# Kernel tuning notes

Measured on AMD Instinct MI355X. Metric: run time of the kernel, lower is better.

Reference implementation:

```python
import jax, jax.numpy as jnp
import numpy as np

B, M, N, D = 1, 128, 256, 256   # batch, msa rows, residues, node dim
DE = 128                        # edge (pair) dim
H, DH = 8, 64                   # heads, dim_head
INNER = H * DH


def setup_inputs() -> dict:
    key = jax.random.key(0)
    ks = jax.random.split(key, 10)
    s = 0.02
    return {
        "x": jax.random.normal(ks[0], (B, M, N, D), jnp.float32),
        "edges": jax.random.normal(ks[1], (B, N, N, DE), jnp.float32),
        "mask": jnp.ones((B, M, N), dtype=bool),
        "ln_g": jnp.ones((D,), jnp.float32),
        "ln_b": jnp.zeros((D,), jnp.float32),
        "Wq": jax.random.normal(ks[2], (D, INNER), jnp.float32) * s,
        "Wkv": jax.random.normal(ks[3], (D, 2 * INNER), jnp.float32) * s,
        "Wg": jax.random.normal(ks[4], (D, INNER), jnp.float32) * s,
        "bg": jnp.ones((INNER,), jnp.float32),
        "Wo": jax.random.normal(ks[5], (INNER, D), jnp.float32) * s,
        "bo": jnp.zeros((D,), jnp.float32),
        "Wb": jax.random.normal(ks[6], (DE, H), jnp.float32) * s,
    }


def reference(x, edges, mask, ln_g, ln_b, Wq, Wkv, Wg, bg, Wo, bo, Wb):
    b, m, n, d = x.shape
    scale = DH ** -0.5
    # LayerNorm over node dim (biased variance, eps=1e-5 as torch default)
    mu = x.mean(-1, keepdims=True)
    var = x.var(-1, keepdims=True)
    xn = (x - mu) / jnp.sqrt(var + 1e-5) * ln_g + ln_b

    # pair bias: [b, h, i, j], shared across MSA rows
    bias = jnp.einsum('bijc,ch->bhij', edges, Wb)

    # projections, split heads: [b, m, n, h, dh]
    q = jnp.einsum('bmnd,de->bmne', xn, Wq).reshape(b, m, n, H, DH) * scale
    kv = jnp.einsum('bmnd,de->bmne', xn, Wkv)
    k = kv[..., :INNER].reshape(b, m, n, H, DH)
    v = kv[..., INNER:].reshape(b, m, n, H, DH)

    # tied queries: mean over MSA rows (global_query_attn, tie_dim=m)
    qm = q.mean(axis=1)  # [b, n, h, dh]
    dots = jnp.einsum('bihd,bmjhd->bmhij', qm, k) + bias[:, None]  # [b,m,h,i,j]

    pair_mask = mask[:, :, None, :, None] & mask[:, :, None, None, :]
    neg = -jnp.finfo(dots.dtype).max
    dots = jnp.where(pair_mask, dots, neg)
    attn = jax.nn.softmax(dots, axis=-1)

    out = jnp.einsum('bmhij,bmjhd->bmihd', attn, v).reshape(b, m, n, INNER)
    gates = jax.nn.sigmoid(jnp.einsum('bmnd,de->bmne', xn, Wg) + bg)
    out = out * gates
    return jnp.einsum('bmne,ed->bmnd', out, Wo) + bo
```

## Files before the change

kernel.cpp:

```cpp
#include <hip/hip_runtime.h>
#include <stdint.h>


#define DEV __device__ __forceinline__

typedef __attribute__((ext_vector_type(8))) short bf16x8;
typedef __attribute__((ext_vector_type(4))) float f32x4;

DEV short f2bf(float f) {
  union { float f; uint32_t u; } v; v.f = f;
  uint32_t r = v.u + 0x7fffu + ((v.u >> 16) & 1u);
  return (short)(r >> 16);
}
DEV float bf2f(short s) {
  union { uint32_t u; float f; } v; v.u = ((uint32_t)(uint16_t)s) << 16;
  return v.f;
}

#define GLDS16(gp, lp) __builtin_amdgcn_global_load_lds( \
    (__attribute__((address_space(1))) void*)(gp),       \
    (__attribute__((address_space(3))) void*)(lp), 16, 0, 0)

__global__ __launch_bounds__(256) void k_ln(const float* __restrict__ x,
                                            const float* __restrict__ g,
                                            const float* __restrict__ b,
                                            short* __restrict__ xn) {
  int wave = threadIdx.x >> 6, lane = threadIdx.x & 63;
  long row = (long)blockIdx.x * 4 + wave;
  const float* xr = x + row * 256;
  float4 v = ((const float4*)xr)[lane];
  float s = v.x + v.y + v.z + v.w;
  float sq = v.x*v.x + v.y*v.y + v.z*v.z + v.w*v.w;
#pragma unroll
  for (int o = 1; o < 64; o <<= 1) { s += __shfl_xor(s, o); sq += __shfl_xor(sq, o); }
  float mu = s * (1.f/256.f);
  float var = sq * (1.f/256.f) - mu*mu;
  float rstd = rsqrtf(var + 1e-5f);
  float4 gg = ((const float4*)g)[lane];
  float4 bb = ((const float4*)b)[lane];
  short4 o4;
  o4.x = f2bf((v.x-mu)*rstd*gg.x + bb.x);
  o4.y = f2bf((v.y-mu)*rstd*gg.y + bb.y);
  o4.z = f2bf((v.z-mu)*rstd*gg.z + bb.z);
  o4.w = f2bf((v.w-mu)*rstd*gg.w + bb.w);
  ((short4*)(xn + row * 256))[lane] = o4;
}

__global__ __launch_bounds__(256) void k_wt(const float* __restrict__ Wq,
                                            const float* __restrict__ Wkv,
                                            const float* __restrict__ Wg,
                                            const float* __restrict__ Wo,
                                            short* __restrict__ WT,
                                            short* __restrict__ WoT) {
  int idx = blockIdx.x * 256 + threadIdx.x;
  if (idx < 2048 * 256) {
    int n = idx >> 8, k = idx & 255;
    float v;
    if (n < 512)       v = Wq[k * 512 + n];
    else if (n < 1536) v = Wkv[k * 1024 + (n - 512)];
    else               v = Wg[k * 512 + (n - 1536)];
    WT[idx] = f2bf(v);
  } else {
    int j = idx - 2048 * 256;
    int k = j & 511;
    WoT[j] = f2bf(Wo[k * 256 + (j >> 9)]);
  }
}

__global__ __launch_bounds__(256) void k_bias(const float* __restrict__ edges,
                                              const float* __restrict__ Wb,
                                              float* __restrict__ biasF) {
  int pair = blockIdx.x * 4 + (threadIdx.x >> 6);
  int lane = threadIdx.x & 63;
  const float* e = edges + (long)pair * 128;
  float a0 = e[lane], a1 = e[lane + 64];
  float acc[8];
#pragma unroll
  for (int h = 0; h < 8; ++h)
    acc[h] = a0 * Wb[lane * 8 + h] + a1 * Wb[(lane + 64) * 8 + h];
#pragma unroll
  for (int o = 1; o < 64; o <<= 1) {
#pragma unroll
    for (int h = 0; h < 8; ++h) acc[h] += __shfl_xor(acc[h], o);
  }
  if (lane == 0) {
    int i = pair >> 8, j = pair & 255;
    long base = ((long)(i >> 4) * 16 + (j >> 4)) * 256 +
                (((i >> 2) & 3) * 16 + (j & 15)) * 4 + (i & 3);
#pragma unroll
    for (int h = 0; h < 8; ++h) biasF[(long)h * 65536 + base] = acc[h];
  }
}

__global__ __launch_bounds__(1024) void k_xbar(const short* __restrict__ xn,
                                               float* __restrict__ xbar) {
  __shared__ float red[3][256];
  int i = blockIdx.x;
  int d = threadIdx.x & 255, mc = threadIdx.x >> 8;
  const short* p = xn + (long)mc * 32 * 65536 + (long)i * 256 + d;
  float s = 0.f;
#pragma unroll 8
  for (int mm = 0; mm < 32; ++mm) s += bf2f(p[(long)mm * 65536]);
  if (mc) red[mc - 1][d] = s;
  __syncthreads();
  if (mc == 0)
    xbar[i * 256 + d] = (s + red[0][d] + red[1][d] + red[2][d]) * (1.f / 128.f);
}

__global__ __launch_bounds__(512) void k_qmg(const float* __restrict__ xbar,
                                             const short* __restrict__ WT,
                                             short* __restrict__ qm) {
  int i = blockIdx.x;
  int e = threadIdx.x;
  const float* xb = xbar + i * 256;
  float acc = 0.f;
  for (int d = 0; d < 256; d += 8) {
    bf16x8 w = *(const bf16x8*)&WT[e * 256 + d];
#pragma unroll
    for (int t = 0; t < 8; ++t) acc += xb[d + t] * bf2f(w[t]);
  }
  qm[((e >> 6) * 256 + i) * 64 + (e & 63)] = f2bf(acc * 0.125f);
}

__global__ __launch_bounds__(512, 4) void k_attn(const short* __restrict__ xn,
                                                 const short* __restrict__ WT,
                                                 const short* __restrict__ qm,
                                                 const float* __restrict__ biasF,
                                                 const float* __restrict__ bg,
                                                 short* __restrict__ outA) {
  __shared__ short kL[256 * 64];
  __shared__ short vL[64 * 256];
  __shared__ short pL[8 * 16 * 64];
  int h = blockIdx.x, m = blockIdx.y;
  int tid = threadIdx.x;
  int wave = tid >> 6, lane = tid & 63;
  int quad = lane >> 4, l15 = lane & 15;
  int l7 = l15 & 7;

  short* WL = kL;
  int rW0 = tid >> 2;
  int gW0 = ((tid & 3) ^ ((rW0 >> 1) & 3)) * 8;
  int rW1 = (512 + tid) >> 2;
  int gW1 = (((512 + tid) & 3) ^ ((rW1 >> 1) & 3)) * 8;
  long wg0 = ((long)(512 * ((rW0 >> 6) + 1) + h * 64 + (rW0 & 63))) * 256;
  long wg1 = ((long)(512 * ((rW1 >> 6) + 1) + h * 64 + (rW1 & 63))) * 256;

#define WSTAGE(buf, kc) do {                                                   \
    int k0_ = (kc) * 32;                                                       \
    GLDS16(WT + wg0 + k0_ + gW0, &WL[(buf) * 6144 + tid * 8]);                 \
    if (tid < 256) GLDS16(WT + wg1 + k0_ + gW1, &WL[(buf) * 6144 + (512 + tid) * 8]); \
  } while (0)

  const short* xp0 = xn + ((long)m * 256 + wave * 32 + l15) * 256 + quad * 8;
  const short* xp1 = xp0 + 16 * 256;

  f32x4 akT[2][4] = {};
  f32x4 av[2][4] = {};
  f32x4 ag[2][4] = {};

  WSTAGE(0, 0);
  bf16x8 xf[2], xnx[2];
  xf[0] = *(const bf16x8*)xp0;
  xf[1] = *(const bf16x8*)xp1;
  for (int kc = 0; kc < 8; ++kc) {
    int cur = kc & 1;
    __syncthreads();
    if (kc < 7) {
      WSTAGE(1 - cur, kc + 1);
      xnx[0] = *(const bf16x8*)(xp0 + (kc + 1) * 32);
      xnx[1] = *(const bf16x8*)(xp1 + (kc + 1) * 32);
    }
#pragma unroll
    for (int tj = 0; tj < 4; ++tj) {
      int rk = tj * 16 + l15;
      int rv = 64 + rk;
      int rg = 128 + rk;
      bf16x8 wk = *(const bf16x8*)&WL[cur * 6144 + rk * 32 + ((quad ^ ((rk >> 1) & 3)) * 8)];
      bf16x8 wv = *(const bf16x8*)&WL[cur * 6144 + rv * 32 + ((quad ^ ((rv >> 1) & 3)) * 8)];
      bf16x8 wg = *(const bf16x8*)&WL[cur * 6144 + rg * 32 + ((quad ^ ((rg >> 1) & 3)) * 8)];
#pragma unroll
      for (int ti = 0; ti < 2; ++ti) {
        akT[ti][tj] = __builtin_amdgcn_mfma_f32_16x16x32_bf16(wk, xf[ti], akT[ti][tj], 0, 0, 0);
        av[ti][tj]  = __builtin_amdgcn_mfma_f32_16x16x32_bf16(xf[ti], wv, av[ti][tj], 0, 0, 0);
        ag[ti][tj]  = __builtin_amdgcn_mfma_f32_16x16x32_bf16(xf[ti], wg, ag[ti][tj], 0, 0, 0);
      }
    }
    xf[0] = xnx[0]; xf[1] = xnx[1];
  }
  __syncthreads();

#undef WSTAGE

#pragma unroll
  for (int ti = 0; ti < 2; ++ti)
#pragma unroll
    for (int tj = 0; tj < 4; ++tj) {
      int j = wave * 32 + ti * 16 + l15;
      int gd = tj * 2 + (quad >> 1);
      short4 pk;
      pk.x = f2bf(akT[ti][tj][0]); pk.y = f2bf(akT[ti][tj][1]);
      pk.z = f2bf(akT[ti][tj][2]); pk.w = f2bf(akT[ti][tj][3]);
      *(short4*)&kL[j * 64 + ((gd ^ (j & 7)) * 8) + (quad & 1) * 4] = pk;
      int d = tj * 16 + l15;
      int j0 = wave * 32 + ti * 16 + quad * 4;
      int jg = j0 >> 3;
      short4 pv;
      pv.x = f2bf(av[ti][tj][0]); pv.y = f2bf(av[ti][tj][1]);
      pv.z = f2bf(av[ti][tj][2]); pv.w = f2bf(av[ti][tj][3]);
      *(short4*)&vL[d * 256 + ((jg ^ (d & 7)) * 8) + (j0 & 7)] = pv;
    }

  const short* qmh = qm + h * (256 * 64);
  bf16x8 aq[2][2];
#pragma unroll
  for (int ti = 0; ti < 2; ++ti)
#pragma unroll
    for (int ks = 0; ks < 2; ++ks)
      aq[ti][ks] = *(const bf16x8*)&qmh[(wave * 32 + ti * 16 + l15) * 64 + ks * 32 + quad * 8];
  float bgv[4];
#pragma unroll
  for (int td = 0; td < 4; ++td) bgv[td] = bg[h * 64 + td * 16 + l15];

  f32x4 o[2][4] = {};
  float lrow[2][4] = {};
  const float* bF = biasF + ((long)h * 16 + wave * 2) * 16 * 256 + lane * 4;

  __syncthreads();

  for (int jc = 0; jc < 4; ++jc) {
    f32x4 s[2][4];
#pragma unroll
    for (int ti = 0; ti < 2; ++ti)
#pragma unroll
      for (int tj = 0; tj < 4; ++tj)
        s[ti][tj] = *(const f32x4*)&bF[((long)ti * 16 + jc * 4 + tj) * 256];
#pragma unroll
    for (int tj = 0; tj < 4; ++tj) {
      int jrow = jc * 64 + tj * 16 + l15;
      bf16x8 b0 = *(const bf16x8*)&kL[jrow * 64 + ((quad ^ l7) * 8)];
      bf16x8 b1 = *(const bf16x8*)&kL[jrow * 64 + (((4 + quad) ^ l7) * 8)];
#pragma unroll
      for (int ti = 0; ti < 2; ++ti) {
        s[ti][tj] = __builtin_amdgcn_mfma_f32_16x16x32_bf16(aq[ti][0], b0, s[ti][tj], 0, 0, 0);
        s[ti][tj] = __builtin_amdgcn_mfma_f32_16x16x32_bf16(aq[ti][1], b1, s[ti][tj], 0, 0, 0);
      }
    }
#pragma unroll
    for (int ti = 0; ti < 2; ++ti) {
#pragma unroll
      for (int r = 0; r < 4; ++r) {
        int rloc = quad * 4 + r;
#pragma unroll
        for (int tj = 0; tj < 4; ++tj) {
          float p = __expf(s[ti][tj][r]);
          lrow[ti][r] += p;
          int col = tj * 16 + l15;
          int slot = (col >> 3) ^ (rloc & 7);
          pL[wave * 1024 + rloc * 64 + slot * 8 + (col & 7)] = f2bf(p);
        }
      }
      bf16x8 ap0 = *(const bf16x8*)&pL[wave * 1024 + l15 * 64 + ((quad ^ l7) * 8)];
      bf16x8 ap1 = *(const bf16x8*)&pL[wave * 1024 + l15 * 64 + (((4 + quad) ^ l7) * 8)];
#pragma unroll
      for (int td = 0; td < 4; ++td) {
        int drow = td * 16 + l15;
        bf16x8 bv0 = *(const bf16x8*)&vL[drow * 256 + (jc * 8 + (quad ^ l7)) * 8];
        bf16x8 bv1 = *(const bf16x8*)&vL[drow * 256 + (jc * 8 + ((4 + quad) ^ l7)) * 8];
        o[ti][td] = __builtin_amdgcn_mfma_f32_16x16x32_bf16(ap0, bv0, o[ti][td], 0, 0, 0);
        o[ti][td] = __builtin_amdgcn_mfma_f32_16x16x32_bf16(ap1, bv1, o[ti][td], 0, 0, 0);
      }
    }
  }

#pragma unroll
  for (int ti = 0; ti < 2; ++ti)
#pragma unroll
    for (int r = 0; r < 4; ++r) {
      float l = lrow[ti][r];
#pragma unroll
      for (int off = 1; off < 16; off <<= 1) l += __shfl_xor(l, off);
      float inv = 1.f / l;
      int i = wave * 32 + ti * 16 + quad * 4 + r;
      long rowoff = (long)m * 256 + i;
#pragma unroll
      for (int td = 0; td < 4; ++td) {
        int dh = td * 16 + l15;
        float gv = 1.f / (1.f + __expf(-(ag[ti][td][r] + bgv[td])));
        outA[rowoff * 512 + h * 64 + dh] = f2bf(o[ti][td][r] * inv * gv);
      }
    }
}

__global__ __launch_bounds__(256, 3) void k_out(const short* __restrict__ A,
                                                const short* __restrict__ B,
                                                float* __restrict__ out,
                                                const float* __restrict__ bo) {
  __shared__ short As[2][128 * 32];
  __shared__ short Bs[2][128 * 32];
  int tid = threadIdx.x;
  int wave = tid >> 6, lane = tid & 63;
  int quad = lane >> 4, l15 = lane & 15;
  long row0 = (long)blockIdx.y * 128;
  int col0 = blockIdx.x * 128;
  int wi = (wave >> 1) * 64, wj = (wave & 1) * 64;
  f32x4 acc[4][4] = {};
  const short* Ab = A + row0 * 512;
  const short* Bb = B + (long)col0 * 512;
  int r0 = tid >> 2, gc0 = tid & 3;
  int g0 = (gc0 ^ ((r0 >> 1) & 3)) * 8;
  int g1 = (gc0 ^ (((r0 + 64) >> 1) & 3)) * 8;

#define OSTAGE(buf, k0) do {                                          \
    GLDS16(Ab + (long)r0 * 512 + (k0) + g0,        &As[buf][tid * 8]);          \
    GLDS16(Ab + (long)(r0 + 64) * 512 + (k0) + g1, &As[buf][(tid + 256) * 8]);  \
    GLDS16(Bb + (long)r0 * 512 + (k0) + g0,        &Bs[buf][tid * 8]);          \
    GLDS16(Bb + (long)(r0 + 64) * 512 + (k0) + g1, &Bs[buf][(tid + 256) * 8]);  \
  } while (0)

  OSTAGE(0, 0);
  for (int it = 0; it < 16; ++it) {
    int cur = it & 1;
    __syncthreads();
    if (it < 15) OSTAGE(1 - cur, (it + 1) * 32);
    bf16x8 a[4], b[4];
#pragma unroll
    for (int t = 0; t < 4; ++t) {
      int ra = wi + t * 16 + l15;
      int rb = wj + t * 16 + l15;
      a[t] = *(const bf16x8*)&As[cur][ra * 32 + ((quad ^ ((ra >> 1) & 3)) * 8)];
      b[t] = *(const bf16x8*)&Bs[cur][rb * 32 + ((quad ^ ((rb >> 1) & 3)) * 8)];
    }
#pragma unroll
    for (int ti = 0; ti < 4; ++ti)
#pragma unroll
      for (int tj = 0; tj < 4; ++tj)
        acc[ti][tj] = __builtin_amdgcn_mfma_f32_16x16x32_bf16(b[tj], a[ti], acc[ti][tj], 0, 0, 0);
  }
#undef OSTAGE

#pragma unroll
  for (int ti = 0; ti < 4; ++ti)
#pragma unroll
    for (int tj = 0; tj < 4; ++tj) {
      long token = row0 + wi + ti * 16 + l15;
      int gco = col0 + wj + tj * 16 + quad * 4;
      float4 b4 = *(const float4*)&bo[gco];
      float4 r4;
      r4.x = acc[ti][tj][0] + b4.x;
      r4.y = acc[ti][tj][1] + b4.y;
      r4.z = acc[ti][tj][2] + b4.z;
      r4.w = acc[ti][tj][3] + b4.w;
      *(float4*)&out[token * 256 + gco] = r4;
    }
}

extern "C" void kernel_launch(void* const* d_in, const int* in_sizes, int n_in,
                              void* d_out, int out_size, void* d_ws, size_t ws_size,
                              hipStream_t stream) {
  (void)in_sizes; (void)n_in; (void)out_size; (void)ws_size;
  const float* x     = (const float*)d_in[0];
  const float* edges = (const float*)d_in[1];
  const float* ln_g  = (const float*)d_in[3];
  const float* ln_b  = (const float*)d_in[4];
  const float* Wq    = (const float*)d_in[5];
  const float* Wkv   = (const float*)d_in[6];
  const float* Wg    = (const float*)d_in[7];
  const float* bg    = (const float*)d_in[8];
  const float* Wo    = (const float*)d_in[9];
  const float* bo    = (const float*)d_in[10];
  const float* Wb    = (const float*)d_in[11];
  float* out = (float*)d_out;

  char* ws = (char*)d_ws;
  short* xn    = (short*)ws;  ws += 32768L * 256 * 2;
  short* WT    = (short*)ws;  ws += 2048L * 256 * 2;
  short* WoT   = (short*)ws;  ws += 256L * 512 * 2;
  float* biasF = (float*)ws;  ws += 8L * 256 * 256 * 4;
  float* xbar  = (float*)ws;  ws += 256L * 256 * 4;
  short* qmb   = (short*)ws;  ws += 8L * 256 * 64 * 2;
  short* outA  = (short*)ws;  ws += 32768L * 512 * 2;

  k_ln<<<8192, 256, 0, stream>>>(x, ln_g, ln_b, xn);
  k_wt<<<2560, 256, 0, stream>>>(Wq, Wkv, Wg, Wo, WT, WoT);
  k_bias<<<16384, 256, 0, stream>>>(edges, Wb, biasF);
  k_xbar<<<256, 1024, 0, stream>>>(xn, xbar);
  k_qmg<<<256, 512, 0, stream>>>(xbar, WT, qmb);
  k_attn<<<dim3(8, 128), 512, 0, stream>>>(xn, WT, qmb, biasF, bg, outA);
  k_out<<<dim3(2, 256), 256, 0, stream>>>(outA, WoT, out, bo);
}
```

Before: 276.4 us.

## Defer gate projection until after attention to cut live accumulator registers

The gate projection accumulators are no longer computed together with K and V at the start of the attention kernel. They are now computed in a separate pass after the attention loop, using the pL buffer as staging for the gate weights. The score tiles are also processed one query sub-tile at a time, so only four score accumulators are live instead of eight. Both changes reduce register pressure to support the occupancy target. The cost is re-reading the xn rows and an extra pipelined weight-load loop with additional barriers.

```diff
diff --git a/kernel.cpp b/kernel.cpp
--- a/kernel.cpp
+++ b/kernel.cpp
@@ -137,59 +137,45 @@
   int quad = lane >> 4, l15 = lane & 15;
   int l7 = l15 & 7;
 
-  short* WL = kL;
-  int rW0 = tid >> 2;
-  int gW0 = ((tid & 3) ^ ((rW0 >> 1) & 3)) * 8;
-  int rW1 = (512 + tid) >> 2;
-  int gW1 = (((512 + tid) & 3) ^ ((rW1 >> 1) & 3)) * 8;
-  long wg0 = ((long)(512 * ((rW0 >> 6) + 1) + h * 64 + (rW0 & 63))) * 256;
-  long wg1 = ((long)(512 * ((rW1 >> 6) + 1) + h * 64 + (rW1 & 63))) * 256;
-
-#define WSTAGE(buf, kc) do {                                                   \
-    int k0_ = (kc) * 32;                                                       \
-    GLDS16(WT + wg0 + k0_ + gW0, &WL[(buf) * 6144 + tid * 8]);                 \
-    if (tid < 256) GLDS16(WT + wg1 + k0_ + gW1, &WL[(buf) * 6144 + (512 + tid) * 8]); \
-  } while (0)
+  int rW = tid >> 2;
+  int gW = ((tid & 3) ^ ((rW >> 1) & 3)) * 8;
+  long wgA = ((long)(512 * ((rW >> 6) + 1) + h * 64 + (rW & 63))) * 256;
+  long wgB = ((long)(1536 + h * 64 + rW)) * 256;
 
   const short* xp0 = xn + ((long)m * 256 + wave * 32 + l15) * 256 + quad * 8;
   const short* xp1 = xp0 + 16 * 256;
 
   f32x4 akT[2][4] = {};
   f32x4 av[2][4] = {};
-  f32x4 ag[2][4] = {};
-
-  WSTAGE(0, 0);
-  bf16x8 xf[2], xnx[2];
-  xf[0] = *(const bf16x8*)xp0;
-  xf[1] = *(const bf16x8*)xp1;
+
+#define WSTAGE_A(buf, kc) GLDS16(WT + wgA + (kc) * 32 + gW, &kL[(buf) * 4096 + tid * 8])
+
+  WSTAGE_A(0, 0);
+  bf16x8 xf0 = *(const bf16x8*)xp0, xf1 = *(const bf16x8*)xp1;
   for (int kc = 0; kc < 8; ++kc) {
     int cur = kc & 1;
     __syncthreads();
+    bf16x8 xn0, xn1;
     if (kc < 7) {
-      WSTAGE(1 - cur, kc + 1);
-      xnx[0] = *(const bf16x8*)(xp0 + (kc + 1) * 32);
-      xnx[1] = *(const bf16x8*)(xp1 + (kc + 1) * 32);
+      WSTAGE_A(1 - cur, kc + 1);
+      xn0 = *(const bf16x8*)(xp0 + (kc + 1) * 32);
+      xn1 = *(const bf16x8*)(xp1 + (kc + 1) * 32);
     }
 #pragma unroll
     for (int tj = 0; tj < 4; ++tj) {
       int rk = tj * 16 + l15;
       int rv = 64 + rk;
-      int rg = 128 + rk;
-      bf16x8 wk = *(const bf16x8*)&WL[cur * 6144 + rk * 32 + ((quad ^ ((rk >> 1) & 3)) * 8)];
-      bf16x8 wv = *(const bf16x8*)&WL[cur * 6144 + rv * 32 + ((quad ^ ((rv >> 1) & 3)) * 8)];
-      bf16x8 wg = *(const bf16x8*)&WL[cur * 6144 + rg * 32 + ((quad ^ ((rg >> 1) & 3)) * 8)];
-#pragma unroll
-      for (int ti = 0; ti < 2; ++ti) {
-        akT[ti][tj] = __builtin_amdgcn_mfma_f32_16x16x32_bf16(wk, xf[ti], akT[ti][tj], 0, 0, 0);
-        av[ti][tj]  = __builtin_amdgcn_mfma_f32_16x16x32_bf16(xf[ti], wv, av[ti][tj], 0, 0, 0);
-        ag[ti][tj]  = __builtin_amdgcn_mfma_f32_16x16x32_bf16(xf[ti], wg, ag[ti][tj], 0, 0, 0);
-      }
-    }
-    xf[0] = xnx[0]; xf[1] = xnx[1];
-  }
+      bf16x8 wk = *(const bf16x8*)&kL[cur * 4096 + rk * 32 + ((quad ^ ((rk >> 1) & 3)) * 8)];
+      bf16x8 wv = *(const bf16x8*)&kL[cur * 4096 + rv * 32 + ((quad ^ ((rv >> 1) & 3)) * 8)];
+      akT[0][tj] = __builtin_amdgcn_mfma_f32_16x16x32_bf16(wk, xf0, akT[0][tj], 0, 0, 0);
+      akT[1][tj] = __builtin_amdgcn_mfma_f32_16x16x32_bf16(wk, xf1, akT[1][tj], 0, 0, 0);
+      av[0][tj]  = __builtin_amdgcn_mfma_f32_16x16x32_bf16(xf0, wv, av[0][tj], 0, 0, 0);
+      av[1][tj]  = __builtin_amdgcn_mfma_f32_16x16x32_bf16(xf1, wv, av[1][tj], 0, 0, 0);
+    }
+    xf0 = xn0; xf1 = xn1;
+  }
+#undef WSTAGE_A
   __syncthreads();
-
-#undef WSTAGE
 
 #pragma unroll
   for (int ti = 0; ti < 2; ++ti)
@@ -217,9 +203,6 @@
 #pragma unroll
     for (int ks = 0; ks < 2; ++ks)
       aq[ti][ks] = *(const bf16x8*)&qmh[(wave * 32 + ti * 16 + l15) * 64 + ks * 32 + quad * 8];
-  float bgv[4];
-#pragma unroll
-  for (int td = 0; td < 4; ++td) bgv[td] = bg[h * 64 + td * 16 + l15];
 
   f32x4 o[2][4] = {};
   float lrow[2][4] = {};
@@ -228,31 +211,26 @@
   __syncthreads();
 
   for (int jc = 0; jc < 4; ++jc) {
-    f32x4 s[2][4];
-#pragma unroll
-    for (int ti = 0; ti < 2; ++ti)
+#pragma unroll
+    for (int ti = 0; ti < 2; ++ti) {
+      f32x4 s[4];
 #pragma unroll
       for (int tj = 0; tj < 4; ++tj)
-        s[ti][tj] = *(const f32x4*)&bF[((long)ti * 16 + jc * 4 + tj) * 256];
-#pragma unroll
-    for (int tj = 0; tj < 4; ++tj) {
-      int jrow = jc * 64 + tj * 16 + l15;
-      bf16x8 b0 = *(const bf16x8*)&kL[jrow * 64 + ((quad ^ l7) * 8)];
-      bf16x8 b1 = *(const bf16x8*)&kL[jrow * 64 + (((4 + quad) ^ l7) * 8)];
-#pragma unroll
-      for (int ti = 0; ti < 2; ++ti) {
-        s[ti][tj] = __builtin_amdgcn_mfma_f32_16x16x32_bf16(aq[ti][0], b0, s[ti][tj], 0, 0, 0);
-        s[ti][tj] = __builtin_amdgcn_mfma_f32_16x16x32_bf16(aq[ti][1], b1, s[ti][tj], 0, 0, 0);
+        s[tj] = *(const f32x4*)&bF[((long)ti * 16 + jc * 4 + tj) * 256];
+#pragma unroll
+      for (int tj = 0; tj < 4; ++tj) {
+        int jrow = jc * 64 + tj * 16 + l15;
+        bf16x8 b0 = *(const bf16x8*)&kL[jrow * 64 + ((quad ^ l7) * 8)];
+        bf16x8 b1 = *(const bf16x8*)&kL[jrow * 64 + (((4 + quad) ^ l7) * 8)];
+        s[tj] = __builtin_amdgcn_mfma_f32_16x16x32_bf16(aq[ti][0], b0, s[tj], 0, 0, 0);
+        s[tj] = __builtin_amdgcn_mfma_f32_16x16x32_bf16(aq[ti][1], b1, s[tj], 0, 0, 0);
       }
-    }
-#pragma unroll
-    for (int ti = 0; ti < 2; ++ti) {
 #pragma unroll
       for (int r = 0; r < 4; ++r) {
         int rloc = quad * 4 + r;
 #pragma unroll
         for (int tj = 0; tj < 4; ++tj) {
-          float p = __expf(s[ti][tj][r]);
+          float p = __expf(s[tj][r]);
           lrow[ti][r] += p;
           int col = tj * 16 + l15;
           int slot = (col >> 3) ^ (rloc & 7);
@@ -272,6 +250,37 @@
     }
   }
 
+  __syncthreads();
+  f32x4 ag[2][4] = {};
+
+#define WSTAGE_B(buf, kc) do { if (tid < 256) \
+    GLDS16(WT + wgB + (kc) * 32 + gW, &pL[(buf) * 2048 + tid * 8]); } while (0)
+
+  WSTAGE_B(0, 0);
+  xf0 = *(const bf16x8*)xp0; xf1 = *(const bf16x8*)xp1;
+  for (int kc = 0; kc < 8; ++kc) {
+    int cur = kc & 1;
+    __syncthreads();
+    bf16x8 xn0, xn1;
+    if (kc < 7) {
+      WSTAGE_B(1 - cur, kc + 1);
+      xn0 = *(const bf16x8*)(xp0 + (kc + 1) * 32);
+      xn1 = *(const bf16x8*)(xp1 + (kc + 1) * 32);
+    }
+#pragma unroll
+    for (int tj = 0; tj < 4; ++tj) {
+      int rg = tj * 16 + l15;
+      bf16x8 wg = *(const bf16x8*)&pL[cur * 2048 + rg * 32 + ((quad ^ ((rg >> 1) & 3)) * 8)];
+      ag[0][tj] = __builtin_amdgcn_mfma_f32_16x16x32_bf16(xf0, wg, ag[0][tj], 0, 0, 0);
+      ag[1][tj] = __builtin_amdgcn_mfma_f32_16x16x32_bf16(xf1, wg, ag[1][tj], 0, 0, 0);
+    }
+    xf0 = xn0; xf1 = xn1;
+  }
+#undef WSTAGE_B
+
+  float bgv[4];
+#pragma unroll
+  for (int td = 0; td < 4; ++td) bgv[td] = bg[h * 64 + td * 16 + l15];
 #pragma unroll
   for (int ti = 0; ti < 2; ++ti)
 #pragma unroll
```

After: 411.1 us. +48.8%, slower.
